# Kernel tuning notes

Hardware: AMD Instinct MI355X
Metric: run time of the kernel (lower is better)

The kernel has to match this reference:

```python
import jax, jax.numpy as jnp
import numpy as np

N, E, IN_DIM, C = 30000, 300000, 128, 16


def _xavier(key, shape):
    fan_in, fan_out = shape[1], shape[0]
    lim = np.sqrt(6.0 / (fan_in + fan_out))
    return jax.random.uniform(key, shape, jnp.float32, -lim, lim)


def layernorm(x, g, b, eps=1e-5):
    mu = jnp.mean(x, axis=-1, keepdims=True)
    var = jnp.var(x, axis=-1, keepdims=True)
    return (x - mu) * jax.lax.rsqrt(var + eps) * g + b


def setup_inputs() -> dict:
    key = jax.random.key(0)
    ks = jax.random.split(key, 8)
    D9 = C * 9            # 144
    DI = C * (C * 2)      # 512
    return {
        "x": jax.random.normal(ks[0], (N, IN_DIM), jnp.float32),
        "h": jax.random.normal(ks[1], (N, IN_DIM), jnp.float32),
        "local_frames": jax.random.normal(ks[2], (N, 3, 3), jnp.float32),
        "edge_index": jax.random.randint(ks[3], (2, E), 0, N, jnp.int64),
        "batch": jnp.zeros((N,), jnp.int64),
        # tensor_init: Linear(IN_DIM,144) LN SiLU Linear(144,144) LN SiLU
        "W1": _xavier(ks[4], (D9, IN_DIM)), "b1": jnp.zeros((D9,), jnp.float32),
        "g1": jnp.ones((D9,), jnp.float32), "be1": jnp.zeros((D9,), jnp.float32),
        "W2": _xavier(ks[5], (D9, D9)), "b2": jnp.zeros((D9,), jnp.float32),
        "g2": jnp.ones((D9,), jnp.float32), "be2": jnp.zeros((D9,), jnp.float32),
        # tensor_interaction: Linear(2*IN_DIM,512) LN Sigmoid
        "Wi": _xavier(ks[6], (DI, 2 * IN_DIM)), "bi": jnp.zeros((DI,), jnp.float32),
        "gi": jnp.ones((DI,), jnp.float32), "bei": jnp.zeros((DI,), jnp.float32),
    }


def reference(x, h, local_frames, edge_index, batch,
              W1, b1, g1, be1, W2, b2, g2, be2, Wi, bi, gi, bei):
    n = x.shape[0]
    row, col = edge_index[0], edge_index[1]

    # tensor_init(h) -> [N, C, 3, 3]
    t = jax.nn.silu(layernorm(h @ W1.T + b1, g1, be1))
    t = jax.nn.silu(layernorm(t @ W2.T + b2, g2, be2))
    tensors = t.reshape(n, C, 3, 3)

    hi, hj = h[col], h[row]
    ti, tj = tensors[col], tensors[row]
    Ri, Rj = local_frames[col], local_frames[row]

    # R_rel = Ri^T @ Rj : [E,3,3]
    R_rel = jnp.einsum('eki,ekj->eij', Ri, Rj)
    # rotate sender tensor: R_rel T R_rel^T
    tj_in_i = jnp.einsum('eik,eckl,elj->ecij', R_rel, tj, R_rel)

    stacked_tensor = jnp.concatenate([ti, tj_in_i], axis=1)          # [E,2C,3,3]
    stacked_scalars = jnp.concatenate([hi, hj], axis=-1)             # [E,2*IN_DIM]
    w = jax.nn.sigmoid(layernorm(stacked_scalars @ Wi.T + bi, gi, bei))
    int_weights = w.reshape(-1, 2 * C, C)                            # [E,2C,C]

    t_new = jnp.einsum('ekij,ekc->ecij', stacked_tensor, int_weights)  # [E,C,3,3]

    t_out = jax.ops.segment_sum(t_new, col, num_segments=n)           # [N,C,3,3]
    t_out = 0.5 * (t_out + jnp.swapaxes(t_out, -1, -2))
    return t_out
```

## Files before the change

kernel.cpp:

```cpp
#include <hip/hip_runtime.h>

#define NN 30000
#define EE 300000
#define HD 128
#define D9 144

typedef unsigned int uint32;
typedef unsigned short u16;
typedef __attribute__((ext_vector_type(8))) short short8;
typedef __attribute__((ext_vector_type(4))) float f32x4;
typedef __attribute__((ext_vector_type(4))) uint32 u32x4;

__device__ __forceinline__ float sigmoidf_(float x){ return __builtin_amdgcn_rcpf(1.0f + __expf(-x)); }
__device__ __forceinline__ float siluf_(float x){ return x * __builtin_amdgcn_rcpf(1.0f + __expf(-x)); }
__device__ __forceinline__ u16 f2bf(float f){
  uint32 u = __float_as_uint(f);
  return (u16)((u + 0x7fffu + ((u>>16)&1u)) >> 16);
}
__device__ __forceinline__ float bf2f(u16 b){ return __uint_as_float(((uint32)b)<<16); }
__device__ __forceinline__ float bflo(uint32 u){ return __uint_as_float(u<<16); }
__device__ __forceinline__ float bfhi(uint32 u){ return __uint_as_float(u & 0xffff0000u); }
__device__ __forceinline__ uint32 pk2(float a, float b){ return (uint32)f2bf(a) | ((uint32)f2bf(b)<<16); }

__global__ __launch_bounds__(256) void cvt_all_k(
    const float* __restrict__ Wi, u16* __restrict__ Wq,
    const float* __restrict__ W1, u16* __restrict__ W1s,
    const float* __restrict__ W2, u16* __restrict__ W2s,
    const float* __restrict__ gi, const float* __restrict__ bei,
    float* __restrict__ gt, float* __restrict__ bet)
{
  int i = blockIdx.x*256 + threadIdx.x;
  if (i < 512*128){
    int n = i >> 7, k = i & 127;
    float xl = Wi[n*256 + k];
    float xr = Wi[n*256 + 128 + k];
    u16 lh = f2bf(xl);
    Wq[i]          = lh;
    Wq[65536 + i]  = f2bf(xl - bf2f(lh));
    u16 rh = f2bf(xr);
    Wq[131072 + i] = rh;
    Wq[196608 + i] = f2bf(xr - bf2f(rh));
  }
  if (i < 144*128){
    float x = W1[i];
    u16 hh = f2bf(x);
    W1s[i] = hh;
    W1s[18432 + i] = f2bf(x - bf2f(hh));
  }
  if (i < 144*160){
    int r = i / 160, k = i - r*160;
    float x = (k < 144) ? W2[r*144 + k] : 0.f;
    u16 hh = f2bf(x);
    W2s[i] = hh;
    W2s[23040 + i] = f2bf(x - bf2f(hh));
  }
  if (i < 512){
    int c = i & 15, k = i >> 4;
    gt [c*32 + k] = gi[i];
    bet[c*32 + k] = bei[i];
  }
}

__global__ __launch_bounds__(256) void hist_k(const int* __restrict__ ei, uint32* __restrict__ start){
  int e = blockIdx.x*256 + threadIdx.x;
  if (e < EE){
    int col = ei[EE + e];
    col = col < 0 ? 0 : (col >= NN ? NN-1 : col);
    atomicAdd(&start[col], 1u);
  }
}

__global__ __launch_bounds__(1024) void scan_k(uint32* __restrict__ start){
  __shared__ uint32 part[1024];
  const int t = threadIdx.x;
  const int base = t * 30;
  uint32 loc[30];
  uint32 s = 0;
  #pragma unroll
  for (int i = 0; i < 30; ++i){
    int idx = base + i;
    uint32 cv = (idx < NN) ? start[idx] : 0u;
    loc[i] = s;
    s += cv;
  }
  part[t] = s;
  __syncthreads();
  for (int off = 1; off < 1024; off <<= 1){
    uint32 add = (t >= off) ? part[t - off] : 0u;
    __syncthreads();
    part[t] += add;
    __syncthreads();
  }
  uint32 pre = (t == 0) ? 0u : part[t - 1];
  #pragma unroll
  for (int i = 0; i < 30; ++i){
    int idx = base + i;
    if (idx < NN) start[idx] = pre + loc[i];
  }
}

__global__ __launch_bounds__(256) void scatter_k(const int* __restrict__ ei,
                                                 uint32* __restrict__ start,
                                                 u16* __restrict__ srow, u16* __restrict__ scol){
  int e = blockIdx.x*256 + threadIdx.x;
  if (e < EE){
    int row = ei[e];
    row = row < 0 ? 0 : (row >= NN ? NN-1 : row);
    int col = ei[EE + e];
    col = col < 0 ? 0 : (col >= NN ? NN-1 : col);
    uint32 pos = atomicAdd(&start[col], 1u);
    srow[pos] = (u16)row;
    scol[pos] = (u16)col;
  }
}

__global__ __launch_bounds__(256) void node_all_k(
    const float* __restrict__ h, const u16* __restrict__ Wq,
    const float* __restrict__ bi,
    const u16* __restrict__ W1s, const u16* __restrict__ W2s,
    const float* __restrict__ b1, const float* __restrict__ g1, const float* __restrict__ be1,
    const float* __restrict__ b2, const float* __restrict__ g2, const float* __restrict__ be2,
    u16* __restrict__ uu_t, u16* __restrict__ v16_t, float* __restrict__ tens_t)
{
  __shared__ float t1s[16 * 164];
  __shared__ float pool[160];

  const int t = threadIdx.x;
  const int w = t >> 6, l = t & 63, lr = l & 15, lg = l >> 4;
  const int nb = blockIdx.x * 16;
  const int ntile = (w == 0) ? 3 : 2;
  int tiles[3]; tiles[0] = 2*w; tiles[1] = 2*w + 1; tiles[2] = 8;

  short8 aH[4], aL[4];
  {
    const float* qA = h + (size_t)(nb + lr) * HD + lg*8;
    #pragma unroll
    for (int ks = 0; ks < 4; ++ks){
      float4 x0 = *(const float4*)(qA + ks*32);
      float4 x1 = *(const float4*)(qA + ks*32 + 4);
      float xs[8] = {x0.x, x0.y, x0.z, x0.w, x1.x, x1.y, x1.z, x1.w};
      #pragma unroll
      for (int j = 0; j < 8; ++j){
        u16 hh = f2bf(xs[j]);
        aH[ks][j] = (short)hh;
        aL[ks][j] = (short)f2bf(xs[j] - bf2f(hh));
      }
    }
  }

  {
    f32x4 au[8], av[8];
    #pragma unroll
    for (int nt = 0; nt < 8; ++nt){ au[nt] = (f32x4){0,0,0,0}; av[nt] = (f32x4){0,0,0,0}; }
    #pragma unroll
    for (int ks = 0; ks < 4; ++ks){
      #pragma unroll
      for (int nt = 0; nt < 8; ++nt){
        const u16* bu = Wq + (w*128 + nt*16 + lr)*128 + lg*8 + ks*32;
        short8 bH = *(const short8*)bu;
        short8 bL = *(const short8*)(bu + 65536);
        au[nt] = __builtin_amdgcn_mfma_f32_16x16x32_bf16(aH[ks], bH, au[nt], 0, 0, 0);
        au[nt] = __builtin_amdgcn_mfma_f32_16x16x32_bf16(aL[ks], bH, au[nt], 0, 0, 0);
        au[nt] = __builtin_amdgcn_mfma_f32_16x16x32_bf16(aH[ks], bL, au[nt], 0, 0, 0);
        const u16* bv = bu + 131072;
        short8 cH = *(const short8*)bv;
        short8 cL = *(const short8*)(bv + 65536);
        av[nt] = __builtin_amdgcn_mfma_f32_16x16x32_bf16(aH[ks], cH, av[nt], 0, 0, 0);
        av[nt] = __builtin_amdgcn_mfma_f32_16x16x32_bf16(aL[ks], cH, av[nt], 0, 0, 0);
        av[nt] = __builtin_amdgcn_mfma_f32_16x16x32_bf16(aH[ks], cL, av[nt], 0, 0, 0);
      }
    }
    float bb[8];
    #pragma unroll
    for (int nt = 0; nt < 8; ++nt) bb[nt] = bi[w*128 + nt*16 + lr];
    #pragma unroll
    for (int r = 0; r < 4; ++r){
      size_t node = nb + lg*4 + r;
      u32x4 pu;
      pu.x = pk2(au[0][r]+bb[0], au[1][r]+bb[1]);
      pu.y = pk2(au[2][r]+bb[2], au[3][r]+bb[3]);
      pu.z = pk2(au[4][r]+bb[4], au[5][r]+bb[5]);
      pu.w = pk2(au[6][r]+bb[6], au[7][r]+bb[7]);
      *(u32x4*)(uu_t + node*512 + lr*32 + w*8) = pu;
      u32x4 pv;
      pv.x = pk2(av[0][r], av[1][r]); pv.y = pk2(av[2][r], av[3][r]);
      pv.z = pk2(av[4][r], av[5][r]); pv.w = pk2(av[6][r], av[7][r]);
      *(u32x4*)(v16_t + node*512 + lr*32 + w*8) = pv;
    }
  }

  f32x4 acc[3];
  #pragma unroll
  for (int ti = 0; ti < 3; ++ti) acc[ti] = (f32x4){0,0,0,0};
  #pragma unroll
  for (int ks = 0; ks < 4; ++ks){
    for (int ti = 0; ti < ntile; ++ti){
      const u16* b = W1s + (tiles[ti]*16 + lr)*128 + lg*8 + ks*32;
      short8 bH = *(const short8*)b;
      short8 bL = *(const short8*)(b + 18432);
      acc[ti] = __builtin_amdgcn_mfma_f32_16x16x32_bf16(aH[ks], bH, acc[ti], 0, 0, 0);
      acc[ti] = __builtin_amdgcn_mfma_f32_16x16x32_bf16(aL[ks], bH, acc[ti], 0, 0, 0);
      acc[ti] = __builtin_amdgcn_mfma_f32_16x16x32_bf16(aH[ks], bL, acc[ti], 0, 0, 0);
    }
  }
  for (int ti = 0; ti < ntile; ++ti){
    float bb = b1[tiles[ti]*16 + lr];
    #pragma unroll
    for (int r = 0; r < 4; ++r) acc[ti][r] += bb;
  }
  {
    float ps[4], pq[4];
    #pragma unroll
    for (int r = 0; r < 4; ++r){
      float s = 0.f, q = 0.f;
      for (int ti = 0; ti < ntile; ++ti){ s += acc[ti][r]; q += acc[ti][r]*acc[ti][r]; }
      ps[r] = s; pq[r] = q;
    }
    #pragma unroll
    for (int off = 1; off < 16; off <<= 1)
      #pragma unroll
      for (int r = 0; r < 4; ++r){ ps[r] += __shfl_xor(ps[r], off); pq[r] += __shfl_xor(pq[r], off); }
    if (lr == 0){
      #pragma unroll
      for (int r = 0; r < 4; ++r){
        pool[w*32 + (lg*4 + r)*2 + 0] = ps[r];
        pool[w*32 + (lg*4 + r)*2 + 1] = pq[r];
      }
    }
  }
  __syncthreads();
  if (t < 16){
    float s = pool[t*2] + pool[32 + t*2] + pool[64 + t*2] + pool[96 + t*2];
    float q = pool[t*2+1] + pool[32 + t*2+1] + pool[64 + t*2+1] + pool[96 + t*2+1];
    float mu = s * (1.0f/144.0f);
    pool[128 + t] = mu;
    pool[144 + t] = rsqrtf(q * (1.0f/144.0f) - mu*mu + 1e-5f);
  }
  __syncthreads();
  for (int ti = 0; ti < ntile; ++ti){
    int col = tiles[ti]*16 + lr;
    float gg = g1[col], bb = be1[col];
    #pragma unroll
    for (int r = 0; r < 4; ++r){
      int node = lg*4 + r;
      float mu = pool[128 + node], rs = pool[144 + node];
      t1s[node*164 + col] = siluf_((acc[ti][r] - mu) * rs * gg + bb);
    }
  }
  t1s[(t >> 4)*164 + 144 + (t & 15)] = 0.f;
  __syncthreads();

  #pragma unroll
  for (int ti = 0; ti < 3; ++ti) acc[ti] = (f32x4){0,0,0,0};
  #pragma unroll
  for (int ks = 0; ks < 5; ++ks){
    float4 x0 = *(const float4*)&t1s[lr*164 + lg*8 + ks*32];
    float4 x1 = *(const float4*)&t1s[lr*164 + lg*8 + ks*32 + 4];
    float xs[8] = {x0.x, x0.y, x0.z, x0.w, x1.x, x1.y, x1.z, x1.w};
    short8 a2H, a2L;
    #pragma unroll
    for (int j = 0; j < 8; ++j){
      u16 hh = f2bf(xs[j]);
      a2H[j] = (short)hh;
      a2L[j] = (short)f2bf(xs[j] - bf2f(hh));
    }
    for (int ti = 0; ti < ntile; ++ti){
      const u16* b = W2s + (tiles[ti]*16 + lr)*160 + lg*8 + ks*32;
      short8 bH = *(const short8*)b;
      short8 bL = *(const short8*)(b + 23040);
      acc[ti] = __builtin_amdgcn_mfma_f32_16x16x32_bf16(a2H, bH, acc[ti], 0, 0, 0);
      acc[ti] = __builtin_amdgcn_mfma_f32_16x16x32_bf16(a2L, bH, acc[ti], 0, 0, 0);
      acc[ti] = __builtin_amdgcn_mfma_f32_16x16x32_bf16(a2H, bL, acc[ti], 0, 0, 0);
    }
  }
  for (int ti = 0; ti < ntile; ++ti){
    float bb = b2[tiles[ti]*16 + lr];
    #pragma unroll
    for (int r = 0; r < 4; ++r) acc[ti][r] += bb;
  }
  __syncthreads();
  {
    float ps[4], pq[4];
    #pragma unroll
    for (int r = 0; r < 4; ++r){
      float s = 0.f, q = 0.f;
      for (int ti = 0; ti < ntile; ++ti){ s += acc[ti][r]; q += acc[ti][r]*acc[ti][r]; }
      ps[r] = s; pq[r] = q;
    }
    #pragma unroll
    for (int off = 1; off < 16; off <<= 1)
      #pragma unroll
      for (int r = 0; r < 4; ++r){ ps[r] += __shfl_xor(ps[r], off); pq[r] += __shfl_xor(pq[r], off); }
    if (lr == 0){
      #pragma unroll
      for (int r = 0; r < 4; ++r){
        pool[w*32 + (lg*4 + r)*2 + 0] = ps[r];
        pool[w*32 + (lg*4 + r)*2 + 1] = pq[r];
      }
    }
  }
  __syncthreads();
  if (t < 16){
    float s = pool[t*2] + pool[32 + t*2] + pool[64 + t*2] + pool[96 + t*2];
    float q = pool[t*2+1] + pool[32 + t*2+1] + pool[64 + t*2+1] + pool[96 + t*2+1];
    float mu = s * (1.0f/144.0f);
    pool[128 + t] = mu;
    pool[144 + t] = rsqrtf(q * (1.0f/144.0f) - mu*mu + 1e-5f);
  }
  __syncthreads();
  for (int ti = 0; ti < ntile; ++ti){
    int col = tiles[ti]*16 + lr;
    float gg = g2[col], bb = be2[col];
    int c = col / 9, m = col - c*9;
    #pragma unroll
    for (int r = 0; r < 4; ++r){
      int node = lg*4 + r;
      float mu = pool[128 + node], rs = pool[144 + node];
      float val = siluf_((acc[ti][r] - mu) * rs * gg + bb);
      tens_t[(size_t)(nb + node)*144 + m*16 + c] = val;
    }
  }
}

__global__ __launch_bounds__(256) void edge_par_k(
    const u16* __restrict__ uu_t, const u16* __restrict__ v16_t,
    const float* __restrict__ frames, const float* __restrict__ tens_t,
    const float* __restrict__ gt, const float* __restrict__ bet,
    const u16* __restrict__ srow, const u16* __restrict__ scol,
    uint32* __restrict__ tn)
{
  const int t = threadIdx.x;
  const int le = t >> 4, c = t & 15;
  const int e = blockIdx.x*16 + le;
  const int row = (int)srow[e], col = (int)scol[e];

  float z[32];
  {
    const u16* up = uu_t + (size_t)col*512 + c*32;
    const u16* vp = v16_t + (size_t)row*512 + c*32;
    #pragma unroll
    for (int q = 0; q < 4; ++q){
      u32x4 ua = *(const u32x4*)(up + q*8);
      u32x4 va = *(const u32x4*)(vp + q*8);
      z[q*8+0] = bflo(ua.x)+bflo(va.x); z[q*8+1] = bfhi(ua.x)+bfhi(va.x);
      z[q*8+2] = bflo(ua.y)+bflo(va.y); z[q*8+3] = bfhi(ua.y)+bfhi(va.y);
      z[q*8+4] = bflo(ua.z)+bflo(va.z); z[q*8+5] = bfhi(ua.z)+bfhi(va.z);
      z[q*8+6] = bflo(ua.w)+bflo(va.w); z[q*8+7] = bfhi(ua.w)+bfhi(va.w);
    }
  }

  float s = 0.f, q2 = 0.f;
  #pragma unroll
  for (int k = 0; k < 32; ++k){ s += z[k]; q2 += z[k]*z[k]; }
  #pragma unroll
  for (int off = 1; off < 16; off <<= 1){ s += __shfl_xor(s, off); q2 += __shfl_xor(q2, off); }
  float mu = s * (1.0f/512.0f);
  float rs = rsqrtf(q2 * (1.0f/512.0f) - mu*mu + 1e-5f);

  {
    const float* gp = gt  + c*32;
    const float* bp = bet + c*32;
    #pragma unroll
    for (int kq = 0; kq < 8; ++kq){
      float4 g4 = *(const float4*)(gp + kq*4);
      float4 b4 = *(const float4*)(bp + kq*4);
      z[kq*4+0] = sigmoidf_((z[kq*4+0]-mu)*rs*g4.x + b4.x);
      z[kq*4+1] = sigmoidf_((z[kq*4+1]-mu)*rs*g4.y + b4.y);
      z[kq*4+2] = sigmoidf_((z[kq*4+2]-mu)*rs*g4.z + b4.z);
      z[kq*4+3] = sigmoidf_((z[kq*4+3]-mu)*rs*g4.w + b4.w);
    }
  }

  float o[9], G[9];
  {
    const float* ti = tens_t + (size_t)col*144;
    const float* tj = tens_t + (size_t)row*144;
    #pragma unroll
    for (int m = 0; m < 9; ++m){
      float a = 0.f, g = 0.f;
      #pragma unroll
      for (int kq = 0; kq < 4; ++kq){
        float4 t4 = *(const float4*)(ti + m*16 + kq*4);
        a += t4.x*z[kq*4+0] + t4.y*z[kq*4+1] + t4.z*z[kq*4+2] + t4.w*z[kq*4+3];
        float4 u4 = *(const float4*)(tj + m*16 + kq*4);
        g += u4.x*z[16+kq*4+0] + u4.y*z[16+kq*4+1] + u4.z*z[16+kq*4+2] + u4.w*z[16+kq*4+3];
      }
      o[m] = a; G[m] = g;
    }
  }

  {
    const float* Ri = frames + (size_t)col*9;
    const float* Rj = frames + (size_t)row*9;
    float R[9];
    #pragma unroll
    for (int i = 0; i < 3; ++i)
      #pragma unroll
      for (int j = 0; j < 3; ++j)
        R[i*3+j] = Ri[i]*Rj[j] + Ri[3+i]*Rj[3+j] + Ri[6+i]*Rj[6+j];
    float A[9];
    #pragma unroll
    for (int i = 0; i < 3; ++i)
      #pragma unroll
      for (int j = 0; j < 3; ++j)
        A[i*3+j] = R[i*3+0]*G[0+j] + R[i*3+1]*G[3+j] + R[i*3+2]*G[6+j];
    #pragma unroll
    for (int i = 0; i < 3; ++i)
      #pragma unroll
      for (int j = 0; j < 3; ++j)
        o[i*3+j] += A[i*3+0]*R[0+j] + A[i*3+1]*R[3+j] + A[i*3+2]*R[6+j];
  }

  float s01 = 0.5f*(o[1]+o[3]), s02 = 0.5f*(o[2]+o[6]), s12 = 0.5f*(o[5]+o[7]);
  uint32* tp = tn + (size_t)e*48 + c*3;
  tp[0] = pk2(o[0], s01);
  tp[1] = pk2(s02, o[4]);
  tp[2] = pk2(s12, o[8]);
}

__global__ __launch_bounds__(256) void segsum_k(
    const uint32* __restrict__ tn, const uint32* __restrict__ start,
    float* __restrict__ out)
{
  int tid = blockIdx.x*256 + threadIdx.x;
  if (tid >= NN*16) return;
  int n = tid >> 4, c = tid & 15;
  uint32 beg = (n == 0) ? 0u : start[n-1];
  uint32 end = start[n];

  float a0=0.f, a1=0.f, a2=0.f, a3=0.f, a4=0.f, a5=0.f;
  for (uint32 i = beg; i < end; ++i){
    const uint32* tp = tn + (size_t)i*48 + c*3;
    uint32 x0 = tp[0], x1 = tp[1], x2 = tp[2];
    a0 += bflo(x0); a1 += bfhi(x0);
    a2 += bflo(x1); a3 += bfhi(x1);
    a4 += bflo(x2); a5 += bfhi(x2);
  }

  float* op = out + (size_t)n*144 + c*9;
  op[0] = a0; op[1] = a1; op[2] = a2;
  op[3] = a1; op[4] = a3; op[5] = a4;
  op[6] = a2; op[7] = a4; op[8] = a5;
}

extern "C" void kernel_launch(void* const* d_in, const int* in_sizes, int n_in,
                              void* d_out, int out_size, void* d_ws, size_t ws_size,
                              hipStream_t stream) {
    const float* h      = (const float*)d_in[1];
    const float* frames = (const float*)d_in[2];
    const int*   ei     = (const int*)d_in[3];
    const float* W1  = (const float*)d_in[5];
    const float* b1  = (const float*)d_in[6];
    const float* g1  = (const float*)d_in[7];
    const float* be1 = (const float*)d_in[8];
    const float* W2  = (const float*)d_in[9];
    const float* b2  = (const float*)d_in[10];
    const float* g2  = (const float*)d_in[11];
    const float* be2 = (const float*)d_in[12];
    const float* Wi  = (const float*)d_in[13];
    const float* bi  = (const float*)d_in[14];
    const float* gi  = (const float*)d_in[15];
    const float* bei = (const float*)d_in[16];

    float* out = (float*)d_out;

    u16*    uu_t  = (u16*)d_ws;
    u16*    v16_t = (u16*)  ((char*)d_ws + 30720000);
    float*  tens_t= (float*)((char*)d_ws + 61440000);
    u16*    Wq    = (u16*)  ((char*)d_ws + 78720000);
    u16*    W1s   = (u16*)  ((char*)d_ws + 79244288);
    u16*    W2s   = (u16*)  ((char*)d_ws + 79318016);
    float*  gt    = (float*)((char*)d_ws + 79410176);
    float*  bet   = (float*)((char*)d_ws + 79412224);
    uint32* start = (uint32*)((char*)d_ws + 79414272);
    u16*    srow  = (u16*)  ((char*)d_ws + 79534272);
    u16*    scol  = (u16*)  ((char*)d_ws + 80134272);
    uint32* tn    = (uint32*)((char*)d_ws + 80734272);

    hipMemsetAsync(start, 0, NN * sizeof(uint32), stream);

    cvt_all_k<<<256, 256, 0, stream>>>(Wi, Wq, W1, W1s, W2, W2s, gi, bei, gt, bet);
    node_all_k<<<NN/16, 256, 0, stream>>>(h, Wq, bi, W1s, W2s, b1, g1, be1, b2, g2, be2,
                                          uu_t, v16_t, tens_t);
    hist_k<<<(EE + 255)/256, 256, 0, stream>>>(ei, start);
    scan_k<<<1, 1024, 0, stream>>>(start);
    scatter_k<<<(EE + 255)/256, 256, 0, stream>>>(ei, start, srow, scol);
    edge_par_k<<<EE/16, 256, 0, stream>>>(uu_t, v16_t, frames, tens_t, gt, bet, srow, scol, tn);
    segsum_k<<<(NN*16 + 255)/256, 256, 0, stream>>>(tn, start, out);
}
```

Baseline: 631.9 us.

## Split edge work across two half-threads per channel in edge kernel

Each edge now uses 32 threads instead of 16. Each half handles the receiver or the sender 16-weight slice of the interaction weights, and the sender half also applies the frame rotation. The two partial 3x3 results are combined with a shuffle and only one half writes. This halves per-thread register and latency load to raise parallelism and occupancy. The cost is twice as many threads, a duplicated LayerNorm reduction, and idle lanes during the rotation and store.

```diff
diff --git a/kernel.cpp b/kernel.cpp
--- a/kernel.cpp
+++ b/kernel.cpp
@@ -329,17 +329,19 @@
     const u16* __restrict__ srow, const u16* __restrict__ scol,
     uint32* __restrict__ tn)
 {
-  const int t = threadIdx.x;
-  const int le = t >> 4, c = t & 15;
-  const int e = blockIdx.x*16 + le;
+  const int t  = threadIdx.x;
+  const int le = t >> 5;
+  const int hf = (t >> 4) & 1;
+  const int c  = t & 15;
+  const int e  = blockIdx.x*8 + le;
   const int row = (int)srow[e], col = (int)scol[e];
 
-  float z[32];
-  {
-    const u16* up = uu_t + (size_t)col*512 + c*32;
-    const u16* vp = v16_t + (size_t)row*512 + c*32;
-    #pragma unroll
-    for (int q = 0; q < 4; ++q){
+  float z[16];
+  {
+    const u16* up = uu_t  + (size_t)col*512 + c*32 + hf*16;
+    const u16* vp = v16_t + (size_t)row*512 + c*32 + hf*16;
+    #pragma unroll
+    for (int q = 0; q < 2; ++q){
       u32x4 ua = *(const u32x4*)(up + q*8);
       u32x4 va = *(const u32x4*)(vp + q*8);
       z[q*8+0] = bflo(ua.x)+bflo(va.x); z[q*8+1] = bfhi(ua.x)+bfhi(va.x);
@@ -351,17 +353,17 @@
 
   float s = 0.f, q2 = 0.f;
   #pragma unroll
-  for (int k = 0; k < 32; ++k){ s += z[k]; q2 += z[k]*z[k]; }
-  #pragma unroll
-  for (int off = 1; off < 16; off <<= 1){ s += __shfl_xor(s, off); q2 += __shfl_xor(q2, off); }
+  for (int k = 0; k < 16; ++k){ s += z[k]; q2 += z[k]*z[k]; }
+  #pragma unroll
+  for (int off = 1; off < 32; off <<= 1){ s += __shfl_xor(s, off); q2 += __shfl_xor(q2, off); }
   float mu = s * (1.0f/512.0f);
   float rs = rsqrtf(q2 * (1.0f/512.0f) - mu*mu + 1e-5f);
 
   {
-    const float* gp = gt  + c*32;
-    const float* bp = bet + c*32;
-    #pragma unroll
-    for (int kq = 0; kq < 8; ++kq){
+    const float* gp = gt  + c*32 + hf*16;
+    const float* bp = bet + c*32 + hf*16;
+    #pragma unroll
+    for (int kq = 0; kq < 4; ++kq){
       float4 g4 = *(const float4*)(gp + kq*4);
       float4 b4 = *(const float4*)(bp + kq*4);
       z[kq*4+0] = sigmoidf_((z[kq*4+0]-mu)*rs*g4.x + b4.x);
@@ -371,25 +373,23 @@
     }
   }
 
-  float o[9], G[9];
-  {
-    const float* ti = tens_t + (size_t)col*144;
-    const float* tj = tens_t + (size_t)row*144;
+  float P[9];
+  {
+    const float* T = tens_t + (size_t)(hf ? row : col) * 144;
     #pragma unroll
     for (int m = 0; m < 9; ++m){
-      float a = 0.f, g = 0.f;
-      #pragma unroll
-      for (int kq = 0; kq < 4; ++kq){
-        float4 t4 = *(const float4*)(ti + m*16 + kq*4);
-        a += t4.x*z[kq*4+0] + t4.y*z[kq*4+1] + t4.z*z[kq*4+2] + t4.w*z[kq*4+3];
-        float4 u4 = *(const float4*)(tj + m*16 + kq*4);
-        g += u4.x*z[16+kq*4+0] + u4.y*z[16+kq*4+1] + u4.z*z[16+kq*4+2] + u4.w*z[16+kq*4+3];
-      }
-      o[m] = a; G[m] = g;
-    }
-  }
-
-  {
+      float4 a0 = *(const float4*)(T + m*16);
+      float4 a1 = *(const float4*)(T + m*16 + 4);
+      float4 a2 = *(const float4*)(T + m*16 + 8);
+      float4 a3 = *(const float4*)(T + m*16 + 12);
+      P[m] = a0.x*z[0]  + a0.y*z[1]  + a0.z*z[2]  + a0.w*z[3]
+           + a1.x*z[4]  + a1.y*z[5]  + a1.z*z[6]  + a1.w*z[7]
+           + a2.x*z[8]  + a2.y*z[9]  + a2.z*z[10] + a2.w*z[11]
+           + a3.x*z[12] + a3.y*z[13] + a3.z*z[14] + a3.w*z[15];
+    }
+  }
+
+  if (hf){
     const float* Ri = frames + (size_t)col*9;
     const float* Rj = frames + (size_t)row*9;
     float R[9];
@@ -403,19 +403,24 @@
     for (int i = 0; i < 3; ++i)
       #pragma unroll
       for (int j = 0; j < 3; ++j)
-        A[i*3+j] = R[i*3+0]*G[0+j] + R[i*3+1]*G[3+j] + R[i*3+2]*G[6+j];
+        A[i*3+j] = R[i*3+0]*P[0+j] + R[i*3+1]*P[3+j] + R[i*3+2]*P[6+j];
     #pragma unroll
     for (int i = 0; i < 3; ++i)
       #pragma unroll
       for (int j = 0; j < 3; ++j)
-        o[i*3+j] += A[i*3+0]*R[0+j] + A[i*3+1]*R[3+j] + A[i*3+2]*R[6+j];
-  }
-
-  float s01 = 0.5f*(o[1]+o[3]), s02 = 0.5f*(o[2]+o[6]), s12 = 0.5f*(o[5]+o[7]);
-  uint32* tp = tn + (size_t)e*48 + c*3;
-  tp[0] = pk2(o[0], s01);
-  tp[1] = pk2(s02, o[4]);
-  tp[2] = pk2(s12, o[8]);
+        P[i*3+j] = A[i*3+0]*R[0+j] + A[i*3+1]*R[3+j] + A[i*3+2]*R[6+j];
+  }
+
+  #pragma unroll
+  for (int m = 0; m < 9; ++m) P[m] += __shfl_xor(P[m], 16);
+
+  if (hf == 0){
+    float s01 = 0.5f*(P[1]+P[3]), s02 = 0.5f*(P[2]+P[6]), s12 = 0.5f*(P[5]+P[7]);
+    uint32* tp = tn + (size_t)e*48 + c*3;
+    tp[0] = pk2(P[0], s01);
+    tp[1] = pk2(s02, P[4]);
+    tp[2] = pk2(s12, P[8]);
+  }
 }
 
 __global__ __launch_bounds__(256) void segsum_k(
@@ -485,6 +490,6 @@
     hist_k<<<(EE + 255)/256, 256, 0, stream>>>(ei, start);
     scan_k<<<1, 1024, 0, stream>>>(start);
     scatter_k<<<(EE + 255)/256, 256, 0, stream>>>(ei, start, srow, scol);
-    edge_par_k<<<EE/16, 256, 0, stream>>>(uu_t, v16_t, frames, tens_t, gt, bet, srow, scol, tn);
+    edge_par_k<<<EE/8, 256, 0, stream>>>(uu_t, v16_t, frames, tens_t, gt, bet, srow, scol, tn);
     segsum_k<<<(NN*16 + 255)/256, 256, 0, stream>>>(tn, start, out);
 }
```

After: 611.7 us, median of 2. 1.03x faster.
